# Kernel optimization log

Measured on AMD Instinct MI355X. Metric: run time of the kernel, lower is better.

Reference implementation:

```python
import jax, jax.numpy as jnp
import numpy as np

H = 18  # hidden/input size hardcoded in the module
B, T = 1024, 1024

def _uniform(key, shape, scale):
    return jax.random.uniform(key, shape, jnp.float32, -scale, scale)

def setup_inputs() -> dict:
    key = jax.random.key(0)
    ks = jax.random.split(key, 12)
    s = 1.0 / np.sqrt(H)
    x = jax.random.normal(ks[0], (B, T, H), dtype=jnp.float32)
    return {
        "x": x,
        "gru_Wih": _uniform(ks[1], (3 * H, H), s),
        "gru_Whh": _uniform(ks[2], (3 * H, H), s),
        "gru_bih": _uniform(ks[3], (3 * H,), s),
        "gru_bhh": _uniform(ks[4], (3 * H,), s),
        "lstm_Wih": _uniform(ks[5], (4 * H, H), s),
        "lstm_Whh": _uniform(ks[6], (4 * H, H), s),
        "lstm_bih": _uniform(ks[7], (4 * H,), s),
        "lstm_bhh": _uniform(ks[8], (4 * H,), s),
        "fc_W": _uniform(ks[9], (1, H), s),
        "fc_b": _uniform(ks[10], (1,), s),
    }

def _gru(x, Wih, Whh, bih, bhh):
    # x: [B, T, H]. Precompute input contributions for all timesteps.
    xi = jnp.einsum("bth,gh->btg", x, Wih) + bih  # [B, T, 3H]
    xi_t = jnp.transpose(xi, (1, 0, 2))            # [T, B, 3H]
    h0 = jnp.zeros((x.shape[0], H), x.dtype)

    def step(h, xt):
        hh = h @ Whh.T + bhh                        # [B, 3H]
        xr, xz, xn = jnp.split(xt, 3, axis=-1)
        hr, hz, hn = jnp.split(hh, 3, axis=-1)
        r = jax.nn.sigmoid(xr + hr)
        z = jax.nn.sigmoid(xz + hz)
        n = jnp.tanh(xn + r * hn)
        h_new = (1.0 - z) * n + z * h
        return h_new, h_new

    _, hs = jax.lax.scan(step, h0, xi_t)
    return jnp.transpose(hs, (1, 0, 2))             # [B, T, H]

def _lstm(x, Wih, Whh, bih, bhh):
    xi = jnp.einsum("bth,gh->btg", x, Wih) + bih   # [B, T, 4H]
    xi_t = jnp.transpose(xi, (1, 0, 2))
    h0 = jnp.zeros((x.shape[0], H), x.dtype)
    c0 = jnp.zeros((x.shape[0], H), x.dtype)

    def step(carry, xt):
        h, c = carry
        g = xt + h @ Whh.T + bhh                    # [B, 4H]
        i, f, gg, o = jnp.split(g, 4, axis=-1)      # PyTorch gate order i,f,g,o
        i = jax.nn.sigmoid(i)
        f = jax.nn.sigmoid(f)
        gg = jnp.tanh(gg)
        o = jax.nn.sigmoid(o)
        c_new = f * c + i * gg
        h_new = o * jnp.tanh(c_new)
        return (h_new, c_new), h_new

    _, hs = jax.lax.scan(step, (h0, c0), xi_t)
    return jnp.transpose(hs, (1, 0, 2))

def reference(x, gru_Wih, gru_Whh, gru_bih, gru_bhh,
              lstm_Wih, lstm_Whh, lstm_bih, lstm_bhh, fc_W, fc_b):
    g = _gru(x, gru_Wih, gru_Whh, gru_bih, gru_bhh)
    l = _lstm(g, lstm_Wih, lstm_Whh, lstm_bih, lstm_bhh)
    return jnp.einsum("bth,oh->bto", l, fc_W) + fc_b  # [B, T, 1]
```

## Files before the change

### kernel.cpp

```cpp
#include <hip/hip_runtime.h>
#include <cstdint>
#include <cstddef>
#include <math.h>

#define LC 1.44269504088896340736f

__device__ __forceinline__ float rl_(float v, int k) {
    return __int_as_float(__builtin_amdgcn_readlane(__float_as_int(v), k));
}
__device__ __forceinline__ float bp_(float v, int addr4) {
    return __int_as_float(__builtin_amdgcn_ds_bpermute(addr4, __float_as_int(v)));
}
#define SZ_(v, pat) __int_as_float(__builtin_amdgcn_ds_swizzle(__float_as_int(v), (pat)))

__device__ __forceinline__ float sigm_(float u) {
    return __fdividef(1.f, 1.f + exp2f(-LC * u));
}
__device__ __forceinline__ float tanh_(float u) {
    return fmaf(-2.f, __fdividef(1.f, 1.f + exp2f((2.f * LC) * u)), 1.f);
}
__device__ __forceinline__ void ld18_(float* d, const float* s) {
    *(float4*)&d[0]  = *(const float4*)&s[0];
    *(float4*)&d[4]  = *(const float4*)&s[4];
    *(float4*)&d[8]  = *(const float4*)&s[8];
    *(float4*)&d[12] = *(const float4*)&s[12];
    d[16] = s[16]; d[17] = s[17];
}

__global__ __launch_bounds__(128, 2) void rnn_fused7(
    const float* __restrict__ x,
    const float* __restrict__ gWih, const float* __restrict__ gWhh,
    const float* __restrict__ gbih, const float* __restrict__ gbhh,
    const float* __restrict__ lWih, const float* __restrict__ lWhh,
    const float* __restrict__ lbih, const float* __restrict__ lbhh,
    const float* __restrict__ fcW, const float* __restrict__ fcb,
    float* __restrict__ out)
{
    const int tid  = threadIdx.x;
    const int wid  = tid >> 6;
    const int lane = tid & 63;
    const int b    = blockIdx.x;

    __shared__ __align__(16) float ring[32][80];
    __shared__ __align__(16) float xs[2][8][20];

    const float* xb   = x   + (size_t)b * (1024 * 18);
    float*       outp = out + (size_t)b * 1024;

    const bool sec  = (lane >= 54) && (lane < 62);
    const int  rsec = sec ? (64 + lane - 54) : 64;

    if (wid == 0) {
        const int rg = (lane < 54) ? lane : 0;
        float w1[18], w2[18], wX[18];
        #pragma unroll
        for (int k = 0; k < 18; k++) {
            w1[k] = (lane < 54) ? gWhh[rg * 18 + k] : (sec ? lWih[rsec * 18 + k] : 0.f);
            w2[k] = lWih[lane * 18 + k];
            wX[k] = (lane < 54) ? gWih[rg * 18 + k] : 0.f;
        }
        const float bA = (lane < 54) ? gbhh[rg] : (sec ? lbih[rsec] : 0.f);
        const float bP = lbih[lane];
        const float bX = (lane < 54) ? gbih[rg] : 0.f;

        const int i1b = ((lane + 18) & 63) << 2;
        const int i2b = ((lane + 36) & 63) << 2;
        const int i3b = ((lane + 28) & 63) << 2;

        float myh = 0.f;

        const int j0 = lane, j1 = lane + 64, j2 = lane + 128;
        const int r0 = j0 / 18, c0 = j0 % 18;
        const int r1 = j1 / 18, c1 = j1 % 18;
        const int r2 = j2 / 18, c2 = j2 % 18;

        float p0 = xb[j0], p1 = xb[j1], p2 = (lane < 16) ? xb[j2] : 0.f;
        xs[0][r0][c0] = p0; xs[0][r1][c1] = p1; if (lane < 16) xs[0][r2][c2] = p2;
        p0 = xb[144 + j0]; p1 = xb[144 + j1]; if (lane < 16) p2 = xb[144 + j2];

        for (int p = 0; p < 130; p++) {
            __syncthreads();
            if (p < 128) {
                if (p + 1 < 128) {
                    const int bu = (p + 1) & 1;
                    xs[bu][r0][c0] = p0; xs[bu][r1][c1] = p1; if (lane < 16) xs[bu][r2][c2] = p2;
                    if (p + 2 < 128) {
                        const float* xw = xb + (size_t)(p + 2) * 144;
                        p0 = xw[j0]; p1 = xw[j1]; if (lane < 16) p2 = xw[j2];
                    }
                }
                const float* xbase = &xs[p & 1][0][0];
                #pragma unroll 2
                for (int j = 0; j < 8; j++) {
                    const int t = p * 8 + j;
                    float aA0 = bA, aA1 = 0.f, aP0 = bP, aP1 = 0.f;
                    #pragma unroll
                    for (int k = 0; k < 18; k += 2) {
                        const float s0 = rl_(myh, k), s1 = rl_(myh, k + 1);
                        aA0 = fmaf(w1[k],   s0, aA0); aA1 = fmaf(w1[k+1], s1, aA1);
                        aP0 = fmaf(w2[k],   s0, aP0); aP1 = fmaf(w2[k+1], s1, aP1);
                    }
                    const float ha = aA0 + aA1;
                    float* rw = &ring[(t - 1) & 31][0];
                    rw[lane] = aP0 + aP1;
                    if (sec) rw[64 + (lane - 54)] = ha;
                    float xr[18]; ld18_(xr, xbase + j * 20);
                    float xa0 = bX, xa1 = 0.f;
                    #pragma unroll
                    for (int k = 0; k < 18; k += 2) {
                        xa0 = fmaf(wX[k],   xr[k],   xa0);
                        xa1 = fmaf(wX[k+1], xr[k+1], xa1);
                    }
                    const float xa = xa0 + xa1;
                    const float sg = sigm_(xa + ha);
                    const float rv = bp_(sg, i3b);
                    const float tn = tanh_(fmaf(rv, ha, xa));
                    const float zz = bp_(sg, i1b);
                    const float nn = bp_(tn, i2b);
                    const float hnew = fmaf(zz, myh - nn, nn);
                    myh = (lane < 18) ? hnew : myh;
                }
            } else if (p == 128) {
                float aA0 = bA, aA1 = 0.f, aP0 = bP, aP1 = 0.f;
                #pragma unroll
                for (int k = 0; k < 18; k += 2) {
                    const float s0 = rl_(myh, k), s1 = rl_(myh, k + 1);
                    aA0 = fmaf(w1[k],   s0, aA0); aA1 = fmaf(w1[k+1], s1, aA1);
                    aP0 = fmaf(w2[k],   s0, aP0); aP1 = fmaf(w2[k+1], s1, aP1);
                }
                float* rw = &ring[1023 & 31][0];
                rw[lane] = aP0 + aP1;
                if (sec) rw[64 + (lane - 54)] = aA0 + aA1;
            }
        }
    } else {
        float w1[18], w2[18];
        #pragma unroll
        for (int k = 0; k < 18; k++) {
            w1[k] = lWhh[lane * 18 + k];
            w2[k] = sec ? lWhh[rsec * 18 + k] : 0.f;
        }
        const float bB = lbhh[lane];
        const float bS = sec ? lbhh[rsec] : 0.f;

        const int i1b = ((lane + 18) & 63) << 2;
        const int i2b = ((lane + 36) & 63) << 2;
        const int i3b = ((lane + 54) & 63) << 2;
        const int i4b = ((lane + 44) & 63) << 2;

        const bool  isg = (lane >= 36) && (lane < 54);
        const float kl  = isg ? (2.f * LC) : LC;
        const float Aa  = isg ? 2.f : 1.f;
        const float Bb  = isg ? -1.f : 0.f;

        const float fcw  = (lane < 18) ? fcW[lane] : 0.f;
        const float fcbv = fcb[0];

        float myc = 0.f, myhl = 0.f;
        float o0 = 0.f, o1 = 0.f, o2 = 0.f, o3 = 0.f;

        for (int p = 0; p < 130; p++) {
            __syncthreads();
            if (p >= 2) {
                #pragma unroll 2
                for (int j = 0; j < 8; j++) {
                    const int u = (p - 2) * 8 + j;
                    float h0 = bB, h1 = 0.f, g0 = bS, g1 = 0.f;
                    #pragma unroll
                    for (int k = 0; k < 18; k += 2) {
                        const float t0 = rl_(myhl, k), t1 = rl_(myhl, k + 1);
                        h0 = fmaf(w1[k],   t0, h0); h1 = fmaf(w1[k+1], t1, h1);
                        g0 = fmaf(w2[k],   t0, g0); g1 = fmaf(w2[k+1], t1, g1);
                    }
                    const float* rr = &ring[u & 31][0];
                    const float xl  = rr[lane];
                    const float xl2 = rr[64 + ((lane - 54) & 7)];
                    const float a3 = fmaf(Aa, __fdividef(1.f, 1.f + exp2f(-kl * (xl + h0 + h1))), Bb);
                    const float a4 = sigm_(xl2 + g0 + g1);
                    const float ff = bp_(a3, i1b);
                    const float gg = bp_(a3, i2b);
                    const float oa = bp_(a3, i3b);
                    const float ob = bp_(a4, i4b);
                    const float oo = (lane < 10) ? oa : ob;
                    const float cn = fmaf(ff, myc, a3 * gg);
                    myc  = cn;
                    myhl = oo * tanh_(cn);
                    float fv = fcw * myhl;
                    fv += SZ_(fv, 0x041F); fv += SZ_(fv, 0x081F);
                    fv += SZ_(fv, 0x101F); fv += SZ_(fv, 0x201F); fv += SZ_(fv, 0x401F);
                    const float ov = fv + fcbv;
                    const int sm = j & 3;
                    if (sm == 0) o0 = ov; else if (sm == 1) o1 = ov;
                    else if (sm == 2) o2 = ov; else o3 = ov;
                    if (sm == 3 && lane == 0) {
                        float4 vv; vv.x = o0; vv.y = o1; vv.z = o2; vv.w = o3;
                        *reinterpret_cast<float4*>(outp + u - 3) = vv;
                    }
                }
            }
        }
    }
}

extern "C" void kernel_launch(void* const* d_in, const int* in_sizes, int n_in,
                              void* d_out, int out_size, void* d_ws, size_t ws_size,
                              hipStream_t stream)
{
    (void)d_ws; (void)ws_size; (void)in_sizes; (void)n_in; (void)out_size;
    const float* xx   = (const float*)d_in[0];
    const float* gWih = (const float*)d_in[1];
    const float* gWhh = (const float*)d_in[2];
    const float* gbih = (const float*)d_in[3];
    const float* gbhh = (const float*)d_in[4];
    const float* lWih = (const float*)d_in[5];
    const float* lWhh = (const float*)d_in[6];
    const float* lbih = (const float*)d_in[7];
    const float* lbhh = (const float*)d_in[8];
    const float* fcW  = (const float*)d_in[9];
    const float* fcb  = (const float*)d_in[10];
    float* outp = (float*)d_out;

    dim3 grid(1024), block(128);
    hipLaunchKernelGGL(rnn_fused7, grid, block, 0, stream,
                       xx, gWih, gWhh, gbih, gbhh,
                       lWih, lWhh, lbih, lbhh, fcW, fcb, outp);
}
```

Baseline: 571.9 us.

## Split fused GRU/LSTM pipeline into four specialized wavefronts per block

Each block grows from two wavefronts to four, with separate roles: GRU input projection, GRU recurrence, LSTM input projection, and LSTM recurrence. The stages pass data through shared-memory rings and stay in step via block barriers. The aim is to take the input-projection FMAs off the two serial critical paths so each recurrent wave only does its own hidden-state matvec and gates. Role assignment is rotated by block index, which spreads the roles across SIMDs. In exchange it uses more waves and registers per block, and the extra barrier participants may lower occupancy.

Result: no change. 562.7 us (-1.6%).

```diff
diff --git a/kernel.cpp b/kernel.cpp
--- a/kernel.cpp
+++ b/kernel.cpp
@@ -27,7 +27,7 @@
     d[16] = s[16]; d[17] = s[17];
 }
 
-__global__ __launch_bounds__(128, 2) void rnn_fused7(
+__global__ __launch_bounds__(256) void rnn_fused8(
     const float* __restrict__ x,
     const float* __restrict__ gWih, const float* __restrict__ gWhh,
     const float* __restrict__ gbih, const float* __restrict__ gbhh,
@@ -40,34 +40,25 @@
     const int wid  = tid >> 6;
     const int lane = tid & 63;
     const int b    = blockIdx.x;
-
-    __shared__ __align__(16) float ring[32][80];
-    __shared__ __align__(16) float xs[2][8][20];
+    const int role = (wid + b) & 3;
+
+    __shared__ __align__(16) float xaR[16][64];
+    __shared__ __align__(16) float hR [16][64];
+    __shared__ __align__(16) float xlR[16][80];
+    __shared__ __align__(16) float xst[2][8][20];
 
     const float* xb   = x   + (size_t)b * (1024 * 18);
     float*       outp = out + (size_t)b * 1024;
 
     const bool sec  = (lane >= 54) && (lane < 62);
+    const int  rg   = (lane < 54) ? lane : 0;
     const int  rsec = sec ? (64 + lane - 54) : 64;
 
-    if (wid == 0) {
-        const int rg = (lane < 54) ? lane : 0;
-        float w1[18], w2[18], wX[18];
-        #pragma unroll
-        for (int k = 0; k < 18; k++) {
-            w1[k] = (lane < 54) ? gWhh[rg * 18 + k] : (sec ? lWih[rsec * 18 + k] : 0.f);
-            w2[k] = lWih[lane * 18 + k];
-            wX[k] = (lane < 54) ? gWih[rg * 18 + k] : 0.f;
-        }
-        const float bA = (lane < 54) ? gbhh[rg] : (sec ? lbih[rsec] : 0.f);
-        const float bP = lbih[lane];
+    if (role == 3) {
+        float wX[18];
+        #pragma unroll
+        for (int k = 0; k < 18; k++) wX[k] = (lane < 54) ? gWih[rg * 18 + k] : 0.f;
         const float bX = (lane < 54) ? gbih[rg] : 0.f;
-
-        const int i1b = ((lane + 18) & 63) << 2;
-        const int i2b = ((lane + 36) & 63) << 2;
-        const int i3b = ((lane + 28) & 63) << 2;
-
-        float myh = 0.f;
 
         const int j0 = lane, j1 = lane + 64, j2 = lane + 128;
         const int r0 = j0 / 18, c0 = j0 % 18;
@@ -75,73 +66,113 @@
         const int r2 = j2 / 18, c2 = j2 % 18;
 
         float p0 = xb[j0], p1 = xb[j1], p2 = (lane < 16) ? xb[j2] : 0.f;
-        xs[0][r0][c0] = p0; xs[0][r1][c1] = p1; if (lane < 16) xs[0][r2][c2] = p2;
+        xst[0][r0][c0] = p0; xst[0][r1][c1] = p1; if (lane < 16) xst[0][r2][c2] = p2;
+        __builtin_amdgcn_wave_barrier();
+        #pragma unroll
+        for (int j = 0; j < 8; j++) {
+            float xr[18]; ld18_(xr, &xst[0][j][0]);
+            float a0 = bX, a1 = 0.f;
+            #pragma unroll
+            for (int k = 0; k < 18; k += 2) { a0 = fmaf(wX[k], xr[k], a0); a1 = fmaf(wX[k+1], xr[k+1], a1); }
+            xaR[j][lane] = a0 + a1;
+        }
         p0 = xb[144 + j0]; p1 = xb[144 + j1]; if (lane < 16) p2 = xb[144 + j2];
 
         for (int p = 0; p < 130; p++) {
             __syncthreads();
-            if (p < 128) {
-                if (p + 1 < 128) {
-                    const int bu = (p + 1) & 1;
-                    xs[bu][r0][c0] = p0; xs[bu][r1][c1] = p1; if (lane < 16) xs[bu][r2][c2] = p2;
-                    if (p + 2 < 128) {
-                        const float* xw = xb + (size_t)(p + 2) * 144;
-                        p0 = xw[j0]; p1 = xw[j1]; if (lane < 16) p2 = xw[j2];
-                    }
-                }
-                const float* xbase = &xs[p & 1][0][0];
-                #pragma unroll 2
-                for (int j = 0; j < 8; j++) {
-                    const int t = p * 8 + j;
-                    float aA0 = bA, aA1 = 0.f, aP0 = bP, aP1 = 0.f;
+            if (p <= 126) {
+                const int bu = (p + 1) & 1;
+                xst[bu][r0][c0] = p0; xst[bu][r1][c1] = p1; if (lane < 16) xst[bu][r2][c2] = p2;
+                if (p + 2 <= 127) {
+                    const float* xw = xb + (size_t)(p + 2) * 144;
+                    p0 = xw[j0]; p1 = xw[j1]; if (lane < 16) p2 = xw[j2];
+                }
+                __builtin_amdgcn_wave_barrier();
+                const int s1 = ((p + 1) * 8) & 15;
+                #pragma unroll
+                for (int j = 0; j < 8; j++) {
+                    float xr[18]; ld18_(xr, &xst[bu][j][0]);
+                    float a0 = bX, a1 = 0.f;
+                    #pragma unroll
+                    for (int k = 0; k < 18; k += 2) { a0 = fmaf(wX[k], xr[k], a0); a1 = fmaf(wX[k+1], xr[k+1], a1); }
+                    xaR[s1 + j][lane] = a0 + a1;
+                }
+            }
+        }
+    } else if (role == 0) {
+        float wG[18];
+        #pragma unroll
+        for (int k = 0; k < 18; k++) wG[k] = (lane < 54) ? gWhh[rg * 18 + k] : 0.f;
+        const float bG = (lane < 54) ? gbhh[rg] : 0.f;
+
+        const int i1b = ((lane + 18) & 63) << 2;
+        const int i2b = ((lane + 36) & 63) << 2;
+        const int i3b = ((lane + 28) & 63) << 2;
+
+        float myh = 0.f;
+
+        for (int p = 0; p < 130; p++) {
+            __syncthreads();
+            if (p <= 127) {
+                const int s0 = (p * 8) & 15;
+                #pragma unroll
+                for (int j = 0; j < 8; j++) {
+                    const float xa = xaR[s0 + j][lane];
+                    float a0 = bG, a1 = 0.f;
                     #pragma unroll
                     for (int k = 0; k < 18; k += 2) {
-                        const float s0 = rl_(myh, k), s1 = rl_(myh, k + 1);
-                        aA0 = fmaf(w1[k],   s0, aA0); aA1 = fmaf(w1[k+1], s1, aA1);
-                        aP0 = fmaf(w2[k],   s0, aP0); aP1 = fmaf(w2[k+1], s1, aP1);
-                    }
-                    const float ha = aA0 + aA1;
-                    float* rw = &ring[(t - 1) & 31][0];
-                    rw[lane] = aP0 + aP1;
-                    if (sec) rw[64 + (lane - 54)] = ha;
-                    float xr[18]; ld18_(xr, xbase + j * 20);
-                    float xa0 = bX, xa1 = 0.f;
-                    #pragma unroll
-                    for (int k = 0; k < 18; k += 2) {
-                        xa0 = fmaf(wX[k],   xr[k],   xa0);
-                        xa1 = fmaf(wX[k+1], xr[k+1], xa1);
-                    }
-                    const float xa = xa0 + xa1;
+                        const float s_0 = rl_(myh, k), s_1 = rl_(myh, k + 1);
+                        a0 = fmaf(wG[k], s_0, a0); a1 = fmaf(wG[k+1], s_1, a1);
+                    }
+                    const float ha = a0 + a1;
                     const float sg = sigm_(xa + ha);
                     const float rv = bp_(sg, i3b);
                     const float tn = tanh_(fmaf(rv, ha, xa));
                     const float zz = bp_(sg, i1b);
                     const float nn = bp_(tn, i2b);
-                    const float hnew = fmaf(zz, myh - nn, nn);
-                    myh = (lane < 18) ? hnew : myh;
-                }
-            } else if (p == 128) {
-                float aA0 = bA, aA1 = 0.f, aP0 = bP, aP1 = 0.f;
-                #pragma unroll
-                for (int k = 0; k < 18; k += 2) {
-                    const float s0 = rl_(myh, k), s1 = rl_(myh, k + 1);
-                    aA0 = fmaf(w1[k],   s0, aA0); aA1 = fmaf(w1[k+1], s1, aA1);
-                    aP0 = fmaf(w2[k],   s0, aP0); aP1 = fmaf(w2[k+1], s1, aP1);
-                }
-                float* rw = &ring[1023 & 31][0];
-                rw[lane] = aP0 + aP1;
-                if (sec) rw[64 + (lane - 54)] = aA0 + aA1;
+                    myh = fmaf(zz, myh - nn, nn);
+                    hR[s0 + j][lane] = myh;
+                }
+            }
+        }
+    } else if (role == 1) {
+        float wP[18], wS[18];
+        #pragma unroll
+        for (int k = 0; k < 18; k++) {
+            wP[k] = lWih[lane * 18 + k];
+            wS[k] = sec ? lWih[rsec * 18 + k] : 0.f;
+        }
+        const float bP = lbih[lane];
+        const float bS = sec ? lbih[rsec] : 0.f;
+
+        for (int p = 0; p < 130; p++) {
+            __syncthreads();
+            if (p >= 1 && p <= 128) {
+                const int s0 = ((p - 1) * 8) & 15;
+                #pragma unroll
+                for (int j = 0; j < 8; j++) {
+                    const float hreg = hR[s0 + j][lane];
+                    float a0 = bP, a1 = 0.f, c0 = bS, c1 = 0.f;
+                    #pragma unroll
+                    for (int k = 0; k < 18; k += 2) {
+                        const float s_0 = rl_(hreg, k), s_1 = rl_(hreg, k + 1);
+                        a0 = fmaf(wP[k], s_0, a0); a1 = fmaf(wP[k+1], s_1, a1);
+                        c0 = fmaf(wS[k], s_0, c0); c1 = fmaf(wS[k+1], s_1, c1);
+                    }
+                    xlR[s0 + j][lane] = a0 + a1;
+                    if (sec) xlR[s0 + j][64 + (lane - 54)] = c0 + c1;
+                }
             }
         }
     } else {
-        float w1[18], w2[18];
+        float wL[18], wL2[18];
         #pragma unroll
         for (int k = 0; k < 18; k++) {
-            w1[k] = lWhh[lane * 18 + k];
-            w2[k] = sec ? lWhh[rsec * 18 + k] : 0.f;
-        }
-        const float bB = lbhh[lane];
-        const float bS = sec ? lbhh[rsec] : 0.f;
+            wL[k]  = lWhh[lane * 18 + k];
+            wL2[k] = sec ? lWhh[rsec * 18 + k] : 0.f;
+        }
+        const float bL  = lbhh[lane];
+        const float bL2 = sec ? lbhh[rsec] : 0.f;
 
         const int i1b = ((lane + 18) & 63) << 2;
         const int i2b = ((lane + 36) & 63) << 2;
@@ -162,39 +193,37 @@
         for (int p = 0; p < 130; p++) {
             __syncthreads();
             if (p >= 2) {
-                #pragma unroll 2
-                for (int j = 0; j < 8; j++) {
-                    const int u = (p - 2) * 8 + j;
-                    float h0 = bB, h1 = 0.f, g0 = bS, g1 = 0.f;
+                const int base = (p - 2) * 8;
+                const int s0   = base & 15;
+                #pragma unroll
+                for (int j = 0; j < 8; j++) {
+                    const float xl  = xlR[s0 + j][lane];
+                    const float xl2 = xlR[s0 + j][64 + ((lane - 54) & 7)];
+                    float a0 = bL, a1 = 0.f, c0 = bL2, c1 = 0.f;
                     #pragma unroll
                     for (int k = 0; k < 18; k += 2) {
-                        const float t0 = rl_(myhl, k), t1 = rl_(myhl, k + 1);
-                        h0 = fmaf(w1[k],   t0, h0); h1 = fmaf(w1[k+1], t1, h1);
-                        g0 = fmaf(w2[k],   t0, g0); g1 = fmaf(w2[k+1], t1, g1);
-                    }
-                    const float* rr = &ring[u & 31][0];
-                    const float xl  = rr[lane];
-                    const float xl2 = rr[64 + ((lane - 54) & 7)];
-                    const float a3 = fmaf(Aa, __fdividef(1.f, 1.f + exp2f(-kl * (xl + h0 + h1))), Bb);
-                    const float a4 = sigm_(xl2 + g0 + g1);
+                        const float s_0 = rl_(myhl, k), s_1 = rl_(myhl, k + 1);
+                        a0 = fmaf(wL[k], s_0, a0); a1 = fmaf(wL[k+1], s_1, a1);
+                        c0 = fmaf(wL2[k], s_0, c0); c1 = fmaf(wL2[k+1], s_1, c1);
+                    }
+                    const float a3 = fmaf(Aa, __fdividef(1.f, 1.f + exp2f(-kl * (xl + a0 + a1))), Bb);
+                    const float a4 = sigm_(xl2 + c0 + c1);
                     const float ff = bp_(a3, i1b);
                     const float gg = bp_(a3, i2b);
                     const float oa = bp_(a3, i3b);
                     const float ob = bp_(a4, i4b);
                     const float oo = (lane < 10) ? oa : ob;
-                    const float cn = fmaf(ff, myc, a3 * gg);
-                    myc  = cn;
-                    myhl = oo * tanh_(cn);
+                    myc  = fmaf(ff, myc, a3 * gg);
+                    myhl = oo * tanh_(myc);
                     float fv = fcw * myhl;
                     fv += SZ_(fv, 0x041F); fv += SZ_(fv, 0x081F);
                     fv += SZ_(fv, 0x101F); fv += SZ_(fv, 0x201F); fv += SZ_(fv, 0x401F);
                     const float ov = fv + fcbv;
-                    const int sm = j & 3;
-                    if (sm == 0) o0 = ov; else if (sm == 1) o1 = ov;
-                    else if (sm == 2) o2 = ov; else o3 = ov;
-                    if (sm == 3 && lane == 0) {
+                    if ((j & 3) == 0) o0 = ov; else if ((j & 3) == 1) o1 = ov;
+                    else if ((j & 3) == 2) o2 = ov; else o3 = ov;
+                    if ((j & 3) == 3 && lane == 0) {
                         float4 vv; vv.x = o0; vv.y = o1; vv.z = o2; vv.w = o3;
-                        *reinterpret_cast<float4*>(outp + u - 3) = vv;
+                        *reinterpret_cast<float4*>(outp + base + j - 3) = vv;
                     }
                 }
             }
@@ -220,8 +249,8 @@
     const float* fcb  = (const float*)d_in[10];
     float* outp = (float*)d_out;
 
-    dim3 grid(1024), block(128);
-    hipLaunchKernelGGL(rnn_fused7, grid, block, 0, stream,
+    dim3 grid(1024), block(256);
+    hipLaunchKernelGGL(rnn_fused8, grid, block, 0, stream,
                        xx, gWih, gWhh, gbih, gbhh,
                        lWih, lWhh, lbih, lbhh, fcW, fcb, outp);
 }
```
